# Kernel tuning notes

Hardware: AMD Instinct MI355X
Metric: run time of the kernel (lower is better)

## Reference

```python
import jax, jax.numpy as jnp
import numpy as np

B, S, T = 32, 512, 2048
D_TXT, D_MEL = 256, 80


def conv1d(x, w, b, pad):
    # x: (B, C_in, L), w: (C_out, C_in, K)
    y = jax.lax.conv_general_dilated(x, w, window_strides=(1,), padding=[(pad, pad)],
                                     dimension_numbers=('NCH', 'OIH', 'NCH'))
    return y + b[None, :, None]


def text_encoder(x, tw1, tb1, tw2, tb2):
    h = jax.nn.relu(conv1d(x, tw1, tb1, 1))
    return conv1d(h, tw2, tb2, 0)


def mel_encoder(x, mw1, mb1, mw2, mb2, mw3, mb3):
    h = jax.nn.leaky_relu(conv1d(x, mw1, mb1, 1), 0.01)
    h = jax.nn.leaky_relu(conv1d(h, mw2, mb2, 1), 0.01)
    return conv1d(h, mw3, mb3, 0)


def cdist(a, b):
    # a: (B,S,D), b: (B,T,D) -> (B,S,T) euclidean (torch.cdist p=2)
    d2 = (jnp.sum(a * a, -1)[:, :, None] + jnp.sum(b * b, -1)[:, None, :]
          - 2.0 * jnp.einsum('bsd,btd->bst', a, b))
    return jnp.sqrt(jnp.maximum(d2, 1e-12))


def maximum_path(value, mask):
    # Glow-TTS monotonic alignment search. value, mask: (B,S,T) float.
    b, s, t = value.shape
    neg_inf = jnp.float32(-jnp.inf)
    val = (value * mask).transpose(2, 0, 1)  # (T,B,S)
    x_range = jnp.arange(s)

    def fwd_step(v, jc):
        j, col = jc
        v0 = jnp.concatenate([jnp.full((b, 1), neg_inf, v.dtype), v[:, :-1]], axis=1)
        keep = v >= v0  # True: best predecessor is same text index
        v_max = jnp.where(keep, v, v0)
        v_new = jnp.where(x_range[None, :] <= j, v_max + col, neg_inf)
        return v_new, keep

    _, dirs = jax.lax.scan(fwd_step, jnp.zeros((b, s), value.dtype), (jnp.arange(t), val))
    direction = jnp.where(mask.astype(bool), dirs.transpose(1, 2, 0), True).astype(jnp.int32)

    index0 = jnp.sum(mask[:, :, 0], axis=1).astype(jnp.int32) - 1

    def bwd_step(index, dcol):
        row = (jnp.arange(s)[None, :] == index[:, None]).astype(value.dtype)
        d = jnp.take_along_axis(dcol, index[:, None], axis=1)[:, 0]
        return index + d - 1, row

    dcols_rev = jnp.flip(direction, axis=2).transpose(2, 0, 1)  # (T,B,S)
    _, rows = jax.lax.scan(bwd_step, index0, dcols_rev)
    path = jnp.flip(rows, axis=0).transpose(1, 2, 0)  # (B,S,T)
    return path * mask


def setup_inputs() -> dict:
    key = jax.random.key(0)
    ks = jax.random.split(key, 16)
    text = jax.random.normal(ks[0], (B, S, D_TXT), jnp.float32)
    mel = jax.random.normal(ks[1], (B, T, D_MEL), jnp.float32)
    src_len = jax.random.randint(ks[2], (B,), S // 2, S + 1).astype(jnp.int32)
    mel_len = jax.random.randint(ks[3], (B,), T // 2, T + 1).astype(jnp.int32)
    src_mask = jnp.arange(S)[None, :] >= src_len[:, None]   # True = pad
    mel_mask = jnp.arange(T)[None, :] >= mel_len[:, None]
    attn_mask = jnp.zeros((B, S, T), bool)  # unused in forward
    sc = 0.05
    params = dict(
        tw1=jax.random.normal(ks[4], (512, 256, 3)) * sc, tb1=jnp.zeros((512,)),
        tw2=jax.random.normal(ks[5], (80, 512, 1)) * sc, tb2=jnp.zeros((80,)),
        mw1=jax.random.normal(ks[6], (160, 80, 3)) * sc, mb1=jnp.zeros((160,)),
        mw2=jax.random.normal(ks[7], (80, 160, 3)) * sc, mb2=jnp.zeros((80,)),
        mw3=jax.random.normal(ks[8], (80, 80, 1)) * sc, mb3=jnp.zeros((80,)),
    )
    return dict(text=text, mel=mel, src_len=src_len, mel_len=mel_len,
                src_mask=src_mask, mel_mask=mel_mask, attn_mask=attn_mask, **params)


def reference(text, mel, src_len, mel_len, src_mask, mel_mask, attn_mask,
              tw1, tb1, tw2, tb2, mw1, mb1, mw2, mb2, mw3, mb3):
    text_emb = text_encoder(text.transpose(0, 2, 1), tw1, tb1, tw2, tb2).transpose(0, 2, 1)
    mel_emb = mel_encoder(mel.transpose(0, 2, 1), mw1, mb1, mw2, mb2, mw3, mb3).transpose(0, 2, 1)
    text_emb = jnp.where(src_mask[:, :, None], 0.0, text_emb)
    mel_emb = jnp.where(mel_mask[:, :, None], 0.0, mel_emb)
    dist = cdist(text_emb, mel_emb)  # (B,S,T)
    mask1 = jnp.arange(S)[None, :] < src_len[:, None]
    mask2 = jnp.arange(T)[None, :] < mel_len[:, None]
    mask_ST = mask1[:, :, None] & mask2[:, None, :]
    rev = ~mask_ST
    logits = jnp.where(rev, jnp.float32(-1e9), -dist)
    soft_A = jax.nn.softmax(logits, axis=1)  # softmax over text dim
    soft_A = jnp.where(rev, 0.0, soft_A)
    hard_A = maximum_path(soft_A, mask_ST.astype(soft_A.dtype))
    return soft_A, hard_A, rev
```

## Files before the change

kernel.cpp:

```cpp
#include <hip/hip_runtime.h>
#include <hip/hip_bf16.h>
#include <cstdint>

constexpr int NB_ = 32;
constexpr int NS_ = 512;
constexpr int NT_ = 2048;
constexpr int DMEL = 80;

constexpr size_t P = 134217728ull;
constexpr size_t PO_TE   = 0ull;
constexpr size_t PO_ME   = 5242880ull;
constexpr size_t PO_NA   = 26214400ull;
constexpr size_t PO_NB   = 26279936ull;
constexpr size_t PO_W1   = 27066368ull;
constexpr size_t PO_W2   = 28639232ull;
constexpr size_t PO_W3   = 28803072ull;
constexpr size_t PO_W4   = 28956672ull;
constexpr size_t PO_W5   = 29110272ull;
constexpr size_t PO_DIR  = 29139968ull;
constexpr size_t FULL_NEED = P + 33334528ull;

__global__ void k_wtrans(const float* __restrict__ w, float* __restrict__ wT,
                         int CO, int CI, int KW, int total) {
  int id = blockIdx.x * 256 + threadIdx.x;
  if (id >= total) return;
  int co = id % CO;
  int rest = id / CO;
  int ci = rest % CI;
  int tap = rest / CI;
  wT[id] = w[(co * CI + ci) * KW + tap];
}

template <int CIN, int COUT, int NTILE, int NR, int KC, int LOG2L, int ACT,
          bool MASK, bool NORM>
__global__ __launch_bounds__(256) void k_conv(const float* __restrict__ x,
                                              const float* __restrict__ wT,
                                              const float* __restrict__ bias,
                                              float* __restrict__ y,
                                              const int* __restrict__ lenArr,
                                              float* __restrict__ normout) {
  constexpr int L = 1 << LOG2L;
  constexpr int MT = 128;
  constexpr int APAD = 132;
  constexpr int BPAD = NTILE + 4;
  __shared__ float As[KC][APAD];
  __shared__ float Bs[KC][BPAD];

  const int tid = threadIdx.x;
  const int tx = tid & 15;
  const int ty = tid >> 4;
  constexpr int NBLK = COUT / NTILE;
  const int m0 = (blockIdx.x / NBLK) * MT;
  const int n0 = (blockIdx.x % NBLK) * NTILE;

  float acc[8][NR];
#pragma unroll
  for (int i = 0; i < 8; ++i)
#pragma unroll
    for (int j = 0; j < NR; ++j) acc[i][j] = 0.f;

  for (int k0 = 0; k0 < CIN; k0 += KC) {
    __syncthreads();
    constexpr int AF4 = MT * KC / 4;
    constexpr int F4R = KC / 4;
    for (int f = tid; f < AF4; f += 256) {
      int row = f / F4R;
      int ko = (f % F4R) * 4;
      int r = m0 + row;
      float4 v = *reinterpret_cast<const float4*>(&x[(size_t)r * CIN + k0 + ko]);
      As[ko + 0][row] = v.x;
      As[ko + 1][row] = v.y;
      As[ko + 2][row] = v.z;
      As[ko + 3][row] = v.w;
    }
    constexpr int BF4 = KC * NTILE / 4;
    constexpr int BF4R = NTILE / 4;
    for (int f = tid; f < BF4; f += 256) {
      int kk = f / BF4R;
      int no = (f % BF4R) * 4;
      float4 v = *reinterpret_cast<const float4*>(
          &wT[((size_t)(k0 + kk)) * COUT + n0 + no]);
      *reinterpret_cast<float4*>(&Bs[kk][no]) = v;
    }
    __syncthreads();
#pragma unroll 8
    for (int kk = 0; kk < KC; ++kk) {
      float4 a0 = *reinterpret_cast<const float4*>(&As[kk][ty * 8]);
      float4 a1 = *reinterpret_cast<const float4*>(&As[kk][ty * 8 + 4]);
      float av[8] = {a0.x, a0.y, a0.z, a0.w, a1.x, a1.y, a1.z, a1.w};
      float bv[NR];
#pragma unroll
      for (int j = 0; j < NR; ++j) bv[j] = Bs[kk][tx * NR + j];
#pragma unroll
      for (int i = 0; i < 8; ++i)
#pragma unroll
        for (int j = 0; j < NR; ++j) acc[i][j] = fmaf(av[i], bv[j], acc[i][j]);
    }
  }
#pragma unroll
  for (int i = 0; i < 8; ++i) {
    int r = m0 + ty * 8 + i;
    int b = r >> LOG2L;
    int pos = r & (L - 1);
    bool zero = MASK && (pos >= lenArr[b]);
    float sq = 0.f;
#pragma unroll
    for (int j = 0; j < NR; ++j) {
      int c = n0 + tx * NR + j;
      float v = acc[i][j] + bias[c];
      if (ACT == 1) v = fmaxf(v, 0.f);
      if (ACT == 2) v = (v >= 0.f) ? v : 0.01f * v;
      if (zero) v = 0.f;
      y[(size_t)r * COUT + c] = v;
      if (NORM) sq = fmaf(v, v, sq);
    }
    if (NORM) {
      sq += __shfl_xor(sq, 1);
      sq += __shfl_xor(sq, 2);
      sq += __shfl_xor(sq, 4);
      sq += __shfl_xor(sq, 8);
      if (tx == 0) normout[r] = sq;
    }
  }
}

template <int CIN, int COUT, int NTILE, int NR, int KC, int LOG2L, int ACT>
__global__ __launch_bounds__(256) void k_conv3(const float* __restrict__ x,
                                               const float* __restrict__ wT,
                                               const float* __restrict__ bias,
                                               float* __restrict__ y) {
  constexpr int L = 1 << LOG2L;
  constexpr int MT = 128;
  constexpr int MT2 = MT + 2;
  constexpr int APAD = 132;
  constexpr int BPAD = NTILE + 4;
  __shared__ float As[KC][APAD];
  __shared__ float Bs[3][KC][BPAD];

  const int tid = threadIdx.x;
  const int tx = tid & 15;
  const int ty = tid >> 4;
  constexpr int NBLK = COUT / NTILE;
  const int m0 = (blockIdx.x / NBLK) * MT;
  const int n0 = (blockIdx.x % NBLK) * NTILE;
  const bool zlo = (m0 & (L - 1)) == 0;
  const bool zhi = ((m0 + MT) & (L - 1)) == 0;
  constexpr int TOTR = NB_ << LOG2L;

  float acc[8][NR];
#pragma unroll
  for (int i = 0; i < 8; ++i)
#pragma unroll
    for (int j = 0; j < NR; ++j) acc[i][j] = 0.f;

  for (int k0 = 0; k0 < CIN; k0 += KC) {
    __syncthreads();
    constexpr int F4R = KC / 4;
    for (int f = tid; f < MT2 * F4R; f += 256) {
      int h = f / F4R;
      int ko = (f % F4R) * 4;
      int g = m0 + h - 1;
      bool zero = (h == 0 && zlo) || (h == MT + 1 && zhi);
      int gc = g < 0 ? 0 : (g >= TOTR ? TOTR - 1 : g);
      float4 v = *reinterpret_cast<const float4*>(&x[(size_t)gc * CIN + k0 + ko]);
      if (zero) v = make_float4(0.f, 0.f, 0.f, 0.f);
      As[ko + 0][h] = v.x;
      As[ko + 1][h] = v.y;
      As[ko + 2][h] = v.z;
      As[ko + 3][h] = v.w;
    }
    constexpr int BF4R = NTILE / 4;
    for (int f = tid; f < 3 * KC * BF4R; f += 256) {
      int tap = f / (KC * BF4R);
      int rem = f % (KC * BF4R);
      int kk = rem / BF4R;
      int no = (rem % BF4R) * 4;
      float4 v = *reinterpret_cast<const float4*>(
          &wT[((size_t)(tap * CIN + k0 + kk)) * COUT + n0 + no]);
      *reinterpret_cast<float4*>(&Bs[tap][kk][no]) = v;
    }
    __syncthreads();
#pragma unroll 4
    for (int kk = 0; kk < KC; ++kk) {
      float aw[10];
      float4 a0 = *reinterpret_cast<const float4*>(&As[kk][ty * 8]);
      float4 a1 = *reinterpret_cast<const float4*>(&As[kk][ty * 8 + 4]);
      float2 a2 = *reinterpret_cast<const float2*>(&As[kk][ty * 8 + 8]);
      aw[0] = a0.x; aw[1] = a0.y; aw[2] = a0.z; aw[3] = a0.w;
      aw[4] = a1.x; aw[5] = a1.y; aw[6] = a1.z; aw[7] = a1.w;
      aw[8] = a2.x; aw[9] = a2.y;
#pragma unroll
      for (int tap = 0; tap < 3; ++tap) {
        float bv[NR];
#pragma unroll
        for (int j = 0; j < NR; ++j) bv[j] = Bs[tap][kk][tx * NR + j];
#pragma unroll
        for (int i = 0; i < 8; ++i)
#pragma unroll
          for (int j = 0; j < NR; ++j)
            acc[i][j] = fmaf(aw[i + tap], bv[j], acc[i][j]);
      }
    }
  }
#pragma unroll
  for (int i = 0; i < 8; ++i) {
    int r = m0 + ty * 8 + i;
#pragma unroll
    for (int j = 0; j < NR; ++j) {
      int c = n0 + tx * NR + j;
      float v = acc[i][j] + bias[c];
      if (ACT == 1) v = fmaxf(v, 0.f);
      if (ACT == 2) v = (v >= 0.f) ? v : 0.01f * v;
      y[(size_t)r * COUT + c] = v;
    }
  }
}

__global__ __launch_bounds__(256) void k_stats3(
    const float* __restrict__ te, const float* __restrict__ me,
    const float* __restrict__ na, const float* __restrict__ nb,
    const int* __restrict__ src_len, const int* __restrict__ mel_len,
    float* __restrict__ val, float* __restrict__ soft, float* __restrict__ rev) {
  const int b = blockIdx.x >> 5;
  const int t0 = (blockIdx.x & 31) << 6;
  __shared__ float Bt[DMEL][68];
  __shared__ float At[DMEL][68];
  __shared__ float redm[16][64];
  __shared__ float redz[16][64];
  __shared__ float sm[64];
  __shared__ float srz[64];
  __shared__ float pl[64][65];
  const int tid = threadIdx.x;
  for (int f = tid; f < 64 * 20; f += 256) {
    int row = f / 20, ko = (f % 20) << 2;
    float4 v = *reinterpret_cast<const float4*>(
        &me[((size_t)b * NT_ + t0 + row) * DMEL + ko]);
    Bt[ko][row] = v.x; Bt[ko + 1][row] = v.y; Bt[ko + 2][row] = v.z; Bt[ko + 3][row] = v.w;
  }
  const int sy = tid & 15, tx = tid >> 4;
  const int sl = src_len[b], ml = mel_len[b];
  const float NEGINF = -__builtin_inff();
  float nbv[4], mACC[4], zACC[4];
#pragma unroll
  for (int j = 0; j < 4; ++j) {
    nbv[j] = nb[b * NT_ + t0 + (tx << 2) + j];
    mACC[j] = NEGINF;
    zACC[j] = 0.f;
  }
  for (int c = 0; c < 8; ++c) {
    const int s0 = c << 6;
    __syncthreads();
    for (int f = tid; f < 64 * 20; f += 256) {
      int row = f / 20, ko = (f % 20) << 2;
      float4 v = *reinterpret_cast<const float4*>(
          &te[((size_t)b * NS_ + s0 + row) * DMEL + ko]);
      At[ko][row] = v.x; At[ko + 1][row] = v.y; At[ko + 2][row] = v.z; At[ko + 3][row] = v.w;
    }
    __syncthreads();
    float acc[4][4];
#pragma unroll
    for (int i = 0; i < 4; ++i)
#pragma unroll
      for (int j = 0; j < 4; ++j) acc[i][j] = 0.f;
#pragma unroll 8
    for (int kk = 0; kk < DMEL; ++kk) {
      float4 a = *reinterpret_cast<const float4*>(&At[kk][sy << 2]);
      float4 bb = *reinterpret_cast<const float4*>(&Bt[kk][tx << 2]);
      float av[4] = {a.x, a.y, a.z, a.w}, bv[4] = {bb.x, bb.y, bb.z, bb.w};
#pragma unroll
      for (int i = 0; i < 4; ++i)
#pragma unroll
        for (int j = 0; j < 4; ++j) acc[i][j] = fmaf(av[i], bv[j], acc[i][j]);
    }
    float nav[4];
#pragma unroll
    for (int i = 0; i < 4; ++i) nav[i] = na[b * NS_ + s0 + (sy << 2) + i];
#pragma unroll
    for (int j = 0; j < 4; ++j) {
      const int t = t0 + (tx << 2) + j;
      const bool tvalid = t < ml;
      float ov[4];
      float mNew = mACC[j];
#pragma unroll
      for (int i = 0; i < 4; ++i) {
        float d2 = (nav[i] + nbv[j]) - 2.0f * acc[i][j];
        float dist = sqrtf(fmaxf(d2, 1e-12f));
        bool valid = ((s0 + (sy << 2) + i) < sl) && tvalid;
        ov[i] = valid ? -dist : -1e9f;
        mNew = fmaxf(mNew, ov[i]);
      }
      float scale = expf(mACC[j] - mNew);
      float zadd = 0.f;
#pragma unroll
      for (int i = 0; i < 4; ++i) zadd += expf(ov[i] - mNew);
      zACC[j] = zACC[j] * scale + zadd;
      mACC[j] = mNew;
      float4 o = make_float4(ov[0], ov[1], ov[2], ov[3]);
      *reinterpret_cast<float4*>(&val[((size_t)b * NT_ + t) * NS_ + s0 + (sy << 2)]) = o;
    }
  }
#pragma unroll
  for (int j = 0; j < 4; ++j) {
    redm[sy][(tx << 2) + j] = mACC[j];
    redz[sy][(tx << 2) + j] = zACC[j];
  }
  __syncthreads();
  if (tid < 64) {
    float M = NEGINF, Z = 0.f;
#pragma unroll
    for (int y = 0; y < 16; ++y) {
      float m = redm[y][tid], z = redz[y][tid];
      float Mn = fmaxf(M, m);
      Z = Z * expf(M - Mn) + z * expf(m - Mn);
      M = Mn;
    }
    sm[tid] = M;
    srz[tid] = 1.0f / Z;
  }
  __syncthreads();

  const int lane = tid & 63, w = tid >> 6;
  for (int c = 0; c < 8; ++c) {
    const int s0 = c << 6;
#pragma unroll
    for (int j = 0; j < 4; ++j) {
      const int tl = (tx << 2) + j;
      const int t = t0 + tl;
      const bool tvalid = t < ml;
      const float mv = sm[tl];
      const float rzv = srz[tl];
      float* vp = &val[((size_t)b * NT_ + t) * NS_ + s0 + (sy << 2)];
      float4 ov = *reinterpret_cast<const float4*>(vp);
      float4 p;
      p.x = tvalid ? expf(ov.x - mv) * rzv : 0.f;
      p.y = tvalid ? expf(ov.y - mv) * rzv : 0.f;
      p.z = tvalid ? expf(ov.z - mv) * rzv : 0.f;
      p.w = tvalid ? expf(ov.w - mv) * rzv : 0.f;
      *reinterpret_cast<float4*>(vp) = p;
      pl[tl][(sy << 2) + 0] = p.x;
      pl[tl][(sy << 2) + 1] = p.y;
      pl[tl][(sy << 2) + 2] = p.z;
      pl[tl][(sy << 2) + 3] = p.w;
    }
    __syncthreads();
#pragma unroll 4
    for (int i = 0; i < 16; ++i) {
      const int s_loc = (w << 4) + i;
      const int s = s0 + s_loc;
      float p = pl[lane][s_loc];
      size_t o = ((size_t)b * NS_ + s) * NT_ + t0 + lane;
      soft[o] = p;
      bool r = (s >= sl) || ((t0 + lane) >= ml);
      rev[o] = r ? 1.0f : 0.0f;
    }
    __syncthreads();
  }
}

__device__ __forceinline__ float dp_shr1(float x) {
  int r = __builtin_amdgcn_update_dpp(0, __float_as_int(x), 0x138, 0xF, 0xF, true);
  return __int_as_float(r);
}

__device__ __forceinline__ void dp_bar() {
  asm volatile("s_waitcnt lgkmcnt(0)" ::: "memory");
  __builtin_amdgcn_sched_barrier(0);
  __builtin_amdgcn_s_barrier();
}

#define DP_CHUNK(MASKED)                                                      \
  _Pragma("unroll")                                                           \
  for (int rb8 = 0; rb8 < 4; ++rb8) {                                         \
    float4 d0[4], d1[4];                                                      \
    _Pragma("unroll")                                                         \
    for (int rr = 0; rr < 4; ++rr) {                                          \
      const float* rp = rowbase + (((rb8 << 2) + rr) << 9);                   \
      d0[rr] = *reinterpret_cast<const float4*>(rp + (lane << 2));            \
      d1[rr] = *reinterpret_cast<const float4*>(rp + 256 + (lane << 2));      \
    }                                                                         \
    _Pragma("unroll")                                                         \
    for (int rr = 0; rr < 4; ++rr) {                                          \
      const int t = tbase + (rb8 << 2) + rr;                                  \
      float cc[8] = {d0[rr].x, d0[rr].y, d0[rr].z, d0[rr].w,                  \
                     d1[rr].x, d1[rr].y, d1[rr].z, d1[rr].w};                 \
      const int sh = t & 31;                                                  \
      if (t < ml) {                                                           \
        float up = dp_shr1(v[7]);                                             \
        float prev = (lane == 0) ? NEGINF : up;                               \
        _Pragma("unroll")                                                     \
        for (int j = 0; j < 8; ++j) {                                         \
          float cur = v[j];                                                   \
          bool keep = cur >= prev;                                            \
          float vm = fmaxf(cur, prev);                                        \
          float vn;                                                           \
          if (MASKED) {                                                       \
            int s = (lane << 3) + j;                                          \
            vn = (s <= t) ? vm + cc[j] : NEGINF;                              \
          } else {                                                            \
            vn = vm + cc[j];                                                  \
          }                                                                   \
          uint32_t bit = keep ? 1u : inv[j];                                  \
          bw[j] |= bit << sh;                                                 \
          v[j] = vn;                                                          \
          prev = cur;                                                         \
        }                                                                     \
      } else {                                                                \
        _Pragma("unroll")                                                     \
        for (int j = 0; j < 8; ++j) bw[j] |= 1u << sh;                        \
      }                                                                       \
    }                                                                         \
  }

__global__ __launch_bounds__(192) void k_dp(const float* __restrict__ val,
                                            const int* __restrict__ src_len,
                                            const int* __restrict__ mel_len,
                                            uint32_t* __restrict__ dir) {
  __shared__ float buf[2][16][512];
  const int b = blockIdx.x;
  const int wv = threadIdx.x >> 6;
  const int lane = threadIdx.x & 63;
  const float* base = val + (size_t)b * NT_ * NS_;
  const int sl = src_len[b];
  const int ml = mel_len[b];
  const float NEGINF = -__builtin_inff();
  int ca = ((ml + 31) >> 5) << 1;
  const int C_act = ca > 128 ? 128 : ca;

  float4 ra[8], rb[8];
  const int r0 = (wv - 1) << 3;

  float v[8];
  uint32_t bw[8], inv[8];
#pragma unroll
  for (int j = 0; j < 8; ++j) {
    v[j] = 0.0f;
    bw[j] = 0u;
    int s = (lane << 3) + j;
    inv[j] = (s < sl) ? 0u : 1u;
  }

  if (wv > 0) {
#pragma unroll
    for (int rr = 0; rr < 8; ++rr) {
      const float* g = base + (size_t)(r0 + rr) * NS_;
      ra[rr] = *reinterpret_cast<const float4*>(g + (lane << 3));
      rb[rr] = *reinterpret_cast<const float4*>(g + (lane << 3) + 4);
    }
#pragma unroll
    for (int rr = 0; rr < 8; ++rr) {
      float* l = &buf[0][r0 + rr][0];
      *reinterpret_cast<float4*>(l + (lane << 2)) = ra[rr];
      *reinterpret_cast<float4*>(l + 256 + (lane << 2)) = rb[rr];
    }
#pragma unroll
    for (int rr = 0; rr < 8; ++rr) {
      const float* g = base + (size_t)(16 + r0 + rr) * NS_;
      ra[rr] = *reinterpret_cast<const float4*>(g + (lane << 3));
      rb[rr] = *reinterpret_cast<const float4*>(g + (lane << 3) + 4);
    }
  }
  dp_bar();

  for (int c = 0; c < C_act; ++c) {
    if (wv > 0) {
      if (c + 1 < C_act) {
        const int nb = (c + 1) & 1;
#pragma unroll
        for (int rr = 0; rr < 8; ++rr) {
          float* l = &buf[nb][r0 + rr][0];
          *reinterpret_cast<float4*>(l + (lane << 2)) = ra[rr];
          *reinterpret_cast<float4*>(l + 256 + (lane << 2)) = rb[rr];
        }
      }
      if (c + 2 < C_act) {
        const float* cb = base + ((size_t)(c + 2) * 16 + r0) * NS_;
#pragma unroll
        for (int rr = 0; rr < 8; ++rr) {
          const float* g = cb + (size_t)rr * NS_;
          ra[rr] = *reinterpret_cast<const float4*>(g + (lane << 3));
          rb[rr] = *reinterpret_cast<const float4*>(g + (lane << 3) + 4);
        }
      }
    } else {
      const float* rowbase = &buf[c & 1][0][0];
      const int tbase = c << 4;
      if (c < 32) {
        DP_CHUNK(true)
      } else {
        DP_CHUNK(false)
      }
      if (c & 1) {
        const int c32 = c >> 1;
#pragma unroll
        for (int j = 0; j < 8; ++j) {
          dir[((size_t)(b * NS_) + (lane << 3) + j) * 64 + c32] = bw[j];
          bw[j] = 0u;
        }
      }
    }
    dp_bar();
  }
  if (wv == 0) {
    for (int c32 = C_act >> 1; c32 < 64; ++c32) {
#pragma unroll
      for (int j = 0; j < 8; ++j)
        dir[((size_t)(b * NS_) + (lane << 3) + j) * 64 + c32] = 0xFFFFFFFFu;
    }
  }
}

__global__ __launch_bounds__(256) void k_backtrack(
    const uint32_t* __restrict__ dir, const int* __restrict__ src_len,
    const int* __restrict__ mel_len, float* __restrict__ hard) {
  __shared__ uint32_t dl[NS_ * 64];
  const int b = blockIdx.x, tid = threadIdx.x;
  const uint32_t* db = dir + (size_t)b * NS_ * 64;
  for (int f = tid; f < 8192; f += 256) {
    int s = f >> 4;
    int wo = (f & 15) << 2;
    *reinterpret_cast<uint4*>(&dl[s * 64 + wo]) =
        *reinterpret_cast<const uint4*>(&db[s * 64 + wo]);
  }
  __syncthreads();
  if (tid == 0) {
    const int ml = mel_len[b];
    int idx = src_len[b] - 1;
    if (idx < 0) idx = 0;
    if (idx > NS_ - 1) idx = NS_ - 1;
    int cw = -1, ci = -1;
    uint32_t w = 0;
    for (int t = NT_ - 1; t >= 0; --t) {
      int wi = t >> 5;
      if (wi != cw || idx != ci) {
        w = dl[idx * 64 + wi];
        cw = wi;
        ci = idx;
      }
      if (t < ml) hard[((size_t)(b * NS_) + idx) * NT_ + t] = 1.0f;
      int step = (int)((w >> (t & 31)) & 1) - 1;
      idx += step;
      if (idx < 0) idx = 0;
    }
  }
}

extern "C" void kernel_launch(void* const* d_in, const int* in_sizes, int n_in,
                              void* d_out, int out_size, void* d_ws, size_t ws_size,
                              hipStream_t stream) {
  if (n_in != 17) return;
  if (ws_size < FULL_NEED) return;

  const float* text = (const float*)d_in[0];
  const float* mel = (const float*)d_in[1];
  const int* src_len = (const int*)d_in[2];
  const int* mel_len = (const int*)d_in[3];
  const float* tw1 = (const float*)d_in[7];
  const float* tb1 = (const float*)d_in[8];
  const float* tw2 = (const float*)d_in[9];
  const float* tb2 = (const float*)d_in[10];
  const float* mw1 = (const float*)d_in[11];
  const float* mb1 = (const float*)d_in[12];
  const float* mw2 = (const float*)d_in[13];
  const float* mb2 = (const float*)d_in[14];
  const float* mw3 = (const float*)d_in[15];
  const float* mb3 = (const float*)d_in[16];

  char* w8 = (char*)d_ws;
  float* melh1 = (float*)(w8 + 0);
  float* mh2 = (float*)(w8 + 41943040ull);
  float* texth1 = (float*)(w8 + 62914560ull);
  float* val = (float*)(w8 + 0);

  float* te = (float*)(w8 + P + PO_TE);
  float* me = (float*)(w8 + P + PO_ME);
  float* na = (float*)(w8 + P + PO_NA);
  float* nb = (float*)(w8 + P + PO_NB);
  float* wt1 = (float*)(w8 + P + PO_W1);
  float* wt2 = (float*)(w8 + P + PO_W2);
  float* wt3 = (float*)(w8 + P + PO_W3);
  float* wt4 = (float*)(w8 + P + PO_W4);
  float* wt5 = (float*)(w8 + P + PO_W5);
  uint32_t* dir = (uint32_t*)(w8 + P + PO_DIR);

  float* soft = (float*)d_out;
  float* hard = soft + (size_t)NB_ * NS_ * NT_;
  float* rev = soft + 2 * (size_t)NB_ * NS_ * NT_;

  k_wtrans<<<(512 * 256 * 3 + 255) / 256, 256, 0, stream>>>(tw1, wt1, 512, 256, 3, 512 * 256 * 3);
  k_wtrans<<<(80 * 512 + 255) / 256, 256, 0, stream>>>(tw2, wt2, 80, 512, 1, 80 * 512);
  k_wtrans<<<(160 * 80 * 3 + 255) / 256, 256, 0, stream>>>(mw1, wt3, 160, 80, 3, 160 * 80 * 3);
  k_wtrans<<<(80 * 160 * 3 + 255) / 256, 256, 0, stream>>>(mw2, wt4, 80, 160, 3, 80 * 160 * 3);
  k_wtrans<<<(80 * 80 + 255) / 256, 256, 0, stream>>>(mw3, wt5, 80, 80, 1, 80 * 80);

  k_conv3<80, 160, 80, 5, 16, 11, 2><<<512 * 2, 256, 0, stream>>>(mel, wt3, mb1, melh1);
  k_conv3<160, 80, 80, 5, 32, 11, 2><<<512 * 1, 256, 0, stream>>>(melh1, wt4, mb2, mh2);
  k_conv<80, 80, 80, 5, 16, 11, 0, true, true><<<512 * 1, 256, 0, stream>>>(mh2, wt5, mb3, me, mel_len, nb);
  k_conv3<256, 512, 128, 8, 32, 9, 1><<<128 * 4, 256, 0, stream>>>(text, wt1, tb1, texth1);
  k_conv<512, 80, 80, 5, 32, 9, 0, true, true><<<128 * 1, 256, 0, stream>>>(texth1, wt2, tb2, te, src_len, na);

  hipMemsetAsync(hard, 0, (size_t)NB_ * NS_ * NT_ * 4, stream);

  k_stats3<<<NB_ * 32, 256, 0, stream>>>(te, me, na, nb, src_len, mel_len, val, soft, rev);

  k_dp<<<NB_, 192, 0, stream>>>(val, src_len, mel_len, dir);
  k_backtrack<<<NB_, 256, 0, stream>>>(dir, src_len, mel_len, hard);
}
```

Measured before the change: 1.137 ms.

## Skip stats for fully-masked mel tiles and write dense hard path in backtrack

In k_stats3, blocks whose time tile starts beyond mel_len now write zeros to soft and ones to rev and exit early, skipping the distance GEMM and softmax work. The backtrack kernel records the path index per time step in shared memory, then all threads write the full hard tensor (zeros plus ones on the path) with float4 stores. This removes the separate memset of the hard output. The trade-off is that only 32 blocks now write the whole 128 MB hard tensor, where the memset spread that write across the device, so this may limit bandwidth. The path is also written from one thread's serial walk as before.

```diff
diff --git a/kernel.cpp b/kernel.cpp
--- a/kernel.cpp
+++ b/kernel.cpp
@@ -223,6 +223,24 @@
     float* __restrict__ val, float* __restrict__ soft, float* __restrict__ rev) {
   const int b = blockIdx.x >> 5;
   const int t0 = (blockIdx.x & 31) << 6;
+  const int sl = src_len[b], ml = mel_len[b];
+  const int tid = threadIdx.x;
+  const int lane = tid & 63, w = tid >> 6;
+
+  if (t0 >= ml) {
+    for (int c = 0; c < 8; ++c) {
+      const int s0 = c << 6;
+#pragma unroll 4
+      for (int i = 0; i < 16; ++i) {
+        const int s = s0 + (w << 4) + i;
+        size_t o = ((size_t)b * NS_ + s) * NT_ + t0 + lane;
+        soft[o] = 0.f;
+        rev[o] = 1.f;
+      }
+    }
+    return;
+  }
+
   __shared__ float Bt[DMEL][68];
   __shared__ float At[DMEL][68];
   __shared__ float redm[16][64];
@@ -230,7 +248,6 @@
   __shared__ float sm[64];
   __shared__ float srz[64];
   __shared__ float pl[64][65];
-  const int tid = threadIdx.x;
   for (int f = tid; f < 64 * 20; f += 256) {
     int row = f / 20, ko = (f % 20) << 2;
     float4 v = *reinterpret_cast<const float4*>(
@@ -238,7 +255,6 @@
     Bt[ko][row] = v.x; Bt[ko + 1][row] = v.y; Bt[ko + 2][row] = v.z; Bt[ko + 3][row] = v.w;
   }
   const int sy = tid & 15, tx = tid >> 4;
-  const int sl = src_len[b], ml = mel_len[b];
   const float NEGINF = -__builtin_inff();
   float nbv[4], mACC[4], zACC[4];
 #pragma unroll
@@ -319,7 +335,6 @@
   }
   __syncthreads();
 
-  const int lane = tid & 63, w = tid >> 6;
   for (int c = 0; c < 8; ++c) {
     const int s0 = c << 6;
 #pragma unroll
@@ -513,6 +528,7 @@
     const uint32_t* __restrict__ dir, const int* __restrict__ src_len,
     const int* __restrict__ mel_len, float* __restrict__ hard) {
   __shared__ uint32_t dl[NS_ * 64];
+  __shared__ int plds[NT_];
   const int b = blockIdx.x, tid = threadIdx.x;
   const uint32_t* db = dir + (size_t)b * NS_ * 64;
   for (int f = tid; f < 8192; f += 256) {
@@ -523,7 +539,6 @@
   }
   __syncthreads();
   if (tid == 0) {
-    const int ml = mel_len[b];
     int idx = src_len[b] - 1;
     if (idx < 0) idx = 0;
     if (idx > NS_ - 1) idx = NS_ - 1;
@@ -536,11 +551,30 @@
         cw = wi;
         ci = idx;
       }
-      if (t < ml) hard[((size_t)(b * NS_) + idx) * NT_ + t] = 1.0f;
+      plds[t] = idx;
       int step = (int)((w >> (t & 31)) & 1) - 1;
       idx += step;
       if (idx < 0) idx = 0;
     }
+  }
+  __syncthreads();
+  const int ml = mel_len[b];
+  const int tq = tid << 3;
+  int pv[8];
+  float msk[8];
+#pragma unroll
+  for (int k = 0; k < 8; ++k) {
+    pv[k] = plds[tq + k];
+    msk[k] = (tq + k < ml) ? 1.0f : 0.0f;
+  }
+  float* hb = hard + (size_t)b * NS_ * NT_;
+  for (int s = 0; s < NS_; ++s) {
+    float o[8];
+#pragma unroll
+    for (int k = 0; k < 8; ++k) o[k] = (pv[k] == s) ? msk[k] : 0.0f;
+    float4* dst = reinterpret_cast<float4*>(hb + (size_t)s * NT_ + tq);
+    dst[0] = make_float4(o[0], o[1], o[2], o[3]);
+    dst[1] = make_float4(o[4], o[5], o[6], o[7]);
   }
 }
 
@@ -598,8 +632,6 @@
   k_conv3<256, 512, 128, 8, 32, 9, 1><<<128 * 4, 256, 0, stream>>>(text, wt1, tb1, texth1);
   k_conv<512, 80, 80, 5, 32, 9, 0, true, true><<<128 * 1, 256, 0, stream>>>(texth1, wt2, tb2, te, src_len, na);
 
-  hipMemsetAsync(hard, 0, (size_t)NB_ * NS_ * NT_ * 4, stream);
-
   k_stats3<<<NB_ * 32, 256, 0, stream>>>(te, me, na, nb, src_len, mel_len, val, soft, rev);
 
   k_dp<<<NB_, 192, 0, stream>>>(val, src_len, mel_len, dir);
```

Result: slower. 1.507 ms (+32.6%).
